# Performance work log

Hardware: AMD Instinct MI355X
Metric: run time of the kernel (lower is better)

Reference implementation:

```python
import jax, jax.numpy as jnp
import numpy as np
from jax import lax

ULB_LEN = 50000  # hardcoded ulb_dest_len in Cluster.__init__
EPS = 1e-8       # torch.cosine_similarity eps


def _l2norm(x):
    n = jnp.sqrt(jnp.sum(x * x, axis=-1, keepdims=True))
    return x / jnp.maximum(n, EPS)


def setup_inputs() -> dict:
    key = jax.random.key(0)
    k1, k2, k3, k4, k5 = jax.random.split(key, 5)
    B, C, D, K = 32768, 1000, 256, 16
    return {
        "feature": jax.random.normal(k1, (B, D), dtype=jnp.float32),
        "pred": jax.random.normal(k2, (B, C), dtype=jnp.float32),
        "centroids": jax.random.normal(k3, (C, D), dtype=jnp.float32),
        "pred_top_N": jax.random.uniform(k4, (C, K), dtype=jnp.float32),
        "unlabeled_index": jax.random.randint(k5, (B,), 0, ULB_LEN, dtype=jnp.int64),
    }


def reference(feature, pred, centroids, pred_top_N, unlabeled_index):
    B = feature.shape[0]
    C, K = pred_top_N.shape

    # batched cosine similarity to centroids -> argmax label, max cos
    cos = _l2norm(feature) @ _l2norm(centroids).T          # [B, C]
    label = jnp.argmax(cos, axis=1)                        # [B]
    cos_f = jnp.max(cos, axis=1)                           # [B]

    # confidence scores from softmax(pred)
    scores = jnp.max(jax.nn.softmax(pred, axis=1), axis=1)  # [B]

    # per-class mean / unbiased variance of cos_f (torch.var default unbiased)
    ones = jnp.ones((B,), dtype=cos_f.dtype)
    cnt = jax.ops.segment_sum(ones, label, num_segments=C)
    s1 = jax.ops.segment_sum(cos_f, label, num_segments=C)
    s2 = jax.ops.segment_sum(cos_f * cos_f, label, num_segments=C)
    mean = s1 / jnp.maximum(cnt, 1.0)
    var = (s2 - cnt * mean * mean) / jnp.maximum(cnt - 1.0, 1.0)
    std = jnp.sqrt(jnp.maximum(var, 0.0) + 1e-12)

    # weight[i] = normal(mean, std).pdf(cos_f[i]) if cos_f[i] < mean[label] else 1
    m_i, s_i = mean[label], std[label]
    inv_sqrt_2pi = 1.0 / jnp.sqrt(2.0 * jnp.pi).astype(cos_f.dtype)
    pdf = jnp.exp(-0.5 * ((cos_f - m_i) / s_i) ** 2) * inv_sqrt_2pi / s_i
    weight = jnp.where(cos_f < m_i, pdf, jnp.ones_like(cos_f))

    # sequential top-N scatter-insert into pred_top_N / fake_index
    fake_index = jnp.full((C, K), -1, dtype=jnp.int32)

    def step(carry, xs):
        topN, fidx = carry
        lb, sc, ui = xs
        row = topN[lb]                       # [K]
        mi = jnp.argmin(row)
        mv = row[mi]
        do = sc > mv
        topN = topN.at[lb, mi].set(jnp.where(do, sc, mv))
        fidx = fidx.at[lb, mi].set(jnp.where(do, ui.astype(jnp.int32), fidx[lb, mi]))
        return (topN, fidx), None

    (topN, fidx), _ = lax.scan(
        step, (pred_top_N, fake_index),
        (label, scores, unlabeled_index))

    # selected_label scatter (all samples selected: select==1 everywhere)
    selected_label = jnp.full((ULB_LEN,), -1, dtype=jnp.int32)
    selected_label = selected_label.at[unlabeled_index].set(label.astype(jnp.int32))

    return label.astype(jnp.float32), weight, topN, fidx, selected_label
```

## Files before the change

### kernel.cpp

```cpp
#include <hip/hip_runtime.h>
#include <cstdint>
#include <cstddef>

#define B_N   32768
#define C_N   1000
#define C_PAD 1024
#define D_N   256
#define K_N   16
#define ULB_N 50000
#define NCHUNK 128
#define CAP_L 128

#define OFF_L 0
#define OFF_W 32768
#define OFF_T 65536
#define OFF_F 81536
#define OFF_S 97536

typedef __attribute__((ext_vector_type(8))) short short8;
typedef __attribute__((ext_vector_type(4))) float f32x4;

__device__ __forceinline__ unsigned ordf(float f) {
  unsigned u = __float_as_uint(f);
  return (u & 0x80000000u) ? ~u : (u | 0x80000000u);
}
__device__ __forceinline__ float iordf(unsigned h) {
  unsigned u = (h & 0x80000000u) ? (h & 0x7FFFFFFFu) : ~h;
  return __uint_as_float(u);
}
__device__ __forceinline__ unsigned short f2bf(float f) {
  unsigned u = __float_as_uint(f);
  return (unsigned short)((u + 0x7FFFu + ((u >> 16) & 1u)) >> 16);
}
__device__ __forceinline__ float bf2f(unsigned short h) {
  return __uint_as_float(((unsigned)h) << 16);
}

__global__ void k_init(unsigned long long* keys, float* s1, float* s2,
                       int* cnt, int* besti) {
  int i = blockIdx.x * blockDim.x + threadIdx.x;
  if (i < B_N)  keys[i] = 0ull;
  if (i < C_PAD) { s1[i] = 0.f; s2[i] = 0.f; cnt[i] = 0; }
  if (i < ULB_N) besti[i] = -1;
}

__global__ __launch_bounds__(256) void k_pack(const float* __restrict__ src,
                                              short8* __restrict__ dst,
                                              int mt0, int nreal) {
  __shared__ float s[16][260];
  __shared__ float part[16][16];
  __shared__ float dv[16];
  const int t = threadIdx.x;
  const int mtL = blockIdx.x;
  const int r = t >> 4, c4 = (t & 15) * 4;
  const int grow = (mt0 + mtL) * 16 + r;
  #pragma unroll
  for (int i = 0; i < 4; ++i) {
    float4 v;
    if (grow < nreal) v = *reinterpret_cast<const float4*>(&src[(size_t)grow * D_N + c4 + 64 * i]);
    else { v.x = 0.f; v.y = 0.f; v.z = 0.f; v.w = 0.f; }
    s[r][c4 + 64 * i + 0] = v.x; s[r][c4 + 64 * i + 1] = v.y;
    s[r][c4 + 64 * i + 2] = v.z; s[r][c4 + 64 * i + 3] = v.w;
  }
  __syncthreads();
  {
    int c0 = t & 15;
    float ss = 0.f;
    #pragma unroll
    for (int j = 0; j < 16; ++j) { float x = s[r][c0 + 16 * j]; ss += x * x; }
    part[r][c0] = ss;
  }
  __syncthreads();
  if (t < 16) {
    float ss = 0.f;
    #pragma unroll
    for (int j = 0; j < 16; ++j) ss += part[t][j];
    dv[t] = 1.0f / fmaxf(sqrtf(ss), 1e-8f);
  }
  __syncthreads();
  #pragma unroll
  for (int i = 0; i < 4; ++i) {
    int p = t + 256 * i;
    int si = p >> 6, l = p & 63;
    int mr = l & 15, g = l >> 4;
    int kc = (si & 7) * 32 + g * 8;
    bool lo = si >= 8;
    float di = dv[mr];
    short8 v;
    #pragma unroll
    for (int j = 0; j < 8; ++j) {
      float q = s[mr][kc + j] * di;
      unsigned short hi = f2bf(q);
      unsigned short e = lo ? f2bf(q - bf2f(hi)) : hi;
      v[j] = (short)e;
    }
    dst[(size_t)mtL * 1024 + p] = v;
  }
}

__global__ __launch_bounds__(256, 3) void k_mfma(const short8* __restrict__ Ap,
                                                 const short8* __restrict__ Bp,
                                                 unsigned long long* __restrict__ keys,
                                                 int row0) {
  const int bid = blockIdx.x;
  const int nby = gridDim.x >> 3;
  int byl, bx;
  if ((nby & 63) == 0) {
    int xcd = bid & 7, j = bid >> 3;
    int slab = nby >> 3;
    int grp = j >> 6, jj = j & 63;
    byl = xcd * slab + grp * 8 + (jj & 7);
    bx = jj >> 3;
  } else { byl = bid >> 3; bx = bid & 7; }

  const int w = threadIdx.x >> 6, l = threadIdx.x & 63;
  const int wm = (w & 1) * 64, wn = (w >> 1) * 64;
  const short8* a0 = Ap + (size_t)(byl * 8 + (wm >> 4)) * 1024 + l;
  const short8* b0 = Bp + (size_t)(bx * 8 + (wn >> 4)) * 1024 + l;

  f32x4 acc[4][4];
  #pragma unroll
  for (int i = 0; i < 4; ++i)
    #pragma unroll
    for (int j = 0; j < 4; ++j) { acc[i][j][0] = 0.f; acc[i][j][1] = 0.f; acc[i][j][2] = 0.f; acc[i][j][3] = 0.f; }

  short8 Ah[4], Bh[4], Al[4], Bl[4];
#define MFMA16(fa, fb) { \
    _Pragma("unroll") \
    for (int mi = 0; mi < 4; ++mi) \
      _Pragma("unroll") \
      for (int nj = 0; nj < 4; ++nj) \
        acc[mi][nj] = __builtin_amdgcn_mfma_f32_16x16x32_bf16(fa[mi], fb[nj], acc[mi][nj], 0, 0, 0); }

  #pragma unroll 1
  for (int ks = 0; ks < 8; ++ks) {
    #pragma unroll
    for (int i = 0; i < 4; ++i) Ah[i] = a0[ks * 64 + i * 1024];
    #pragma unroll
    for (int i = 0; i < 4; ++i) Bh[i] = b0[ks * 64 + i * 1024];
    #pragma unroll
    for (int i = 0; i < 4; ++i) Al[i] = a0[(ks + 8) * 64 + i * 1024];
    #pragma unroll
    for (int i = 0; i < 4; ++i) Bl[i] = b0[(ks + 8) * 64 + i * 1024];
    MFMA16(Ah, Bh)
    MFMA16(Al, Bh)
    MFMA16(Ah, Bl)
  }
#undef MFMA16

  const int cb = bx * 128 + wn + (l & 15);
  #pragma unroll
  for (int mi = 0; mi < 4; ++mi) {
    #pragma unroll
    for (int r = 0; r < 4; ++r) {
      float bv = -INFINITY; int bc = 0x7FFFFFFF;
      #pragma unroll
      for (int nj = 0; nj < 4; ++nj) {
        int c = cb + nj * 16;
        float v = acc[mi][nj][r];
        if (c < C_N && v > bv) { bv = v; bc = c; }
      }
      #pragma unroll
      for (int mk = 1; mk < 16; mk <<= 1) {
        float ov = __shfl_xor(bv, mk, 64);
        int oc = __shfl_xor(bc, mk, 64);
        if (ov > bv || (ov == bv && oc < bc)) { bv = ov; bc = oc; }
      }
      if ((l & 15) == 0) {
        unsigned long long kk =
            (((unsigned long long)ordf(bv)) << 32) |
            (unsigned long long)(0xFFFFFFFFu - (unsigned)bc);
        atomicMax(&keys[row0 + byl * 128 + wm + mi * 16 + (l >> 4) * 4 + r], kk);
      }
    }
  }
}

__global__ __launch_bounds__(256) void k_scores(const float* __restrict__ pred,
                                                float* __restrict__ scores) {
  __shared__ float red[8];
  int r = blockIdx.x, t = threadIdx.x;
  const float* row = pred + (size_t)r * C_N;
  float x0 = row[t];
  float x1 = row[256 + t];
  float x2 = row[512 + t];
  bool v3 = (768 + t) < C_N;
  float x3 = v3 ? row[768 + t] : -INFINITY;
  float m = fmaxf(fmaxf(x0, x1), fmaxf(x2, x3));
  #pragma unroll
  for (int mk = 1; mk < 64; mk <<= 1) m = fmaxf(m, __shfl_xor(m, mk, 64));
  int wid = t >> 6, lane = t & 63;
  if (lane == 0) red[wid] = m;
  __syncthreads();
  m = fmaxf(fmaxf(red[0], red[1]), fmaxf(red[2], red[3]));
  float s = expf(x0 - m) + expf(x1 - m) + expf(x2 - m) + (v3 ? expf(x3 - m) : 0.f);
  #pragma unroll
  for (int mk = 1; mk < 64; mk <<= 1) s += __shfl_xor(s, mk, 64);
  __syncthreads();
  if (lane == 0) red[4 + wid] = s;
  __syncthreads();
  if (t == 0) {
    float S = ((red[4] + red[5]) + red[6]) + red[7];
    scores[r] = 1.0f / S;
  }
}

__global__ void k_post(const unsigned long long* __restrict__ keys, const int* __restrict__ ui,
                       int* __restrict__ labels, float* __restrict__ cosf_,
                       float* __restrict__ s1, float* __restrict__ s2, int* __restrict__ cnt,
                       int* __restrict__ besti, float* __restrict__ out) {
  int b = blockIdx.x * blockDim.x + threadIdx.x;
  if (b >= B_N) return;
  unsigned long long k = keys[b];
  int c = (int)(0xFFFFFFFFu - (unsigned)k);
  float f = iordf((unsigned)(k >> 32));
  labels[b] = c;
  cosf_[b] = f;
  out[OFF_L + b] = (float)c;
  atomicAdd(&s1[c], f);
  atomicAdd(&s2[c], f * f);
  atomicAdd(&cnt[c], 1);
  atomicMax(&besti[ui[b]], b);
}

__global__ __launch_bounds__(256) void k_hist_rank(const int* __restrict__ labels,
                                                   unsigned short* __restrict__ lrank,
                                                   unsigned short* __restrict__ hist) {
  __shared__ int lab[256];
  __shared__ unsigned histl[C_PAD];
  int chunk = blockIdx.x, t = threadIdx.x;
  int b = chunk * 256 + t;
  #pragma unroll
  for (int r = 0; r < 4; ++r) histl[t + 256 * r] = 0;
  int c = labels[b];
  lab[t] = c;
  __syncthreads();
  atomicAdd(&histl[c], 1u);
  unsigned rk = 0;
  for (int j = 0; j < t; ++j) rk += (lab[j] == c);
  lrank[b] = (unsigned short)rk;
  __syncthreads();
  #pragma unroll
  for (int r = 0; r < 4; ++r)
    hist[chunk * C_PAD + t + 256 * r] = (unsigned short)histl[t + 256 * r];
}

__global__ void k_prefix(const unsigned short* __restrict__ hist,
                         unsigned short* __restrict__ base,
                         int* __restrict__ class_n) {
  int c = blockIdx.x * 64 + threadIdx.x;
  unsigned run = 0;
  for (int t = 0; t < NCHUNK; ++t) {
    unsigned h = hist[t * C_PAD + c];
    base[t * C_PAD + c] = (unsigned short)run;
    run += h;
  }
  class_n[c] = (int)run;
}

__global__ __launch_bounds__(256) void k_sw(const int* __restrict__ labels,
                                            const unsigned short* __restrict__ lrank,
                                            const unsigned short* __restrict__ base,
                                            const float* __restrict__ scores,
                                            const int* __restrict__ ui,
                                            const float* __restrict__ cosf_,
                                            const float* __restrict__ s1,
                                            const float* __restrict__ s2,
                                            const int* __restrict__ cnt,
                                            float* __restrict__ lists_s,
                                            int* __restrict__ lists_u,
                                            float* __restrict__ out) {
  int b = blockIdx.x * blockDim.x + threadIdx.x;
  if (b >= B_N) return;
  int c = labels[b];
  int chunk = b >> 8;
  int pos = (int)base[chunk * C_PAD + c] + (int)lrank[b];
  if (pos < CAP_L) {
    lists_s[c * CAP_L + pos] = scores[b];
    lists_u[c * CAP_L + pos] = ui[b];
  }
  float n = (float)cnt[c];
  float m = s1[c] / fmaxf(n, 1.0f);
  float var = (s2[c] - n * m * m) / fmaxf(n - 1.0f, 1.0f);
  float sd = sqrtf(fmaxf(var, 0.0f) + 1e-12f);
  float cf = cosf_[b];
  float wgt = 1.0f;
  if (cf < m) {
    float z = (cf - m) / sd;
    const float inv = 0.3989422804014327f;
    wgt = expf(-0.5f * (z * z)) * inv / sd;
  }
  out[OFF_W + b] = wgt;
}

__global__ __launch_bounds__(256) void k_replay(const float* __restrict__ ptn,
                                                const float* __restrict__ lists_s,
                                                const int* __restrict__ lists_u,
                                                const int* __restrict__ class_n,
                                                const int* __restrict__ labels,
                                                const float* __restrict__ scores,
                                                const int* __restrict__ ui,
                                                float* __restrict__ out) {
  int c = blockIdx.x * 4 + (threadIdx.x >> 6);
  int lane = threadIdx.x & 63;
  if (c >= C_N) return;

  float tv[K_N]; int fi[K_N];
  #pragma unroll
  for (int j = 0; j < K_N; ++j) { tv[j] = ptn[c * K_N + j]; fi[j] = -1; }

  auto ins = [&](float s, int u) {
    float mv = tv[0]; int mi = 0;
    #pragma unroll
    for (int j = 1; j < K_N; ++j) { if (tv[j] < mv) { mv = tv[j]; mi = j; } }
    if (s > mv) {
      #pragma unroll
      for (int j = 0; j < K_N; ++j) { if (j == mi) { tv[j] = s; fi[j] = u; } }
    }
  };

  int n = class_n[c];
  if (n <= CAP_L) {
    for (int t0 = 0; t0 < n; t0 += 64) {
      float s = 0.f; int u = 0;
      int idx = t0 + lane;
      if (idx < n) { s = lists_s[c * CAP_L + idx]; u = lists_u[c * CAP_L + idx]; }
      int lim = min(64, n - t0);
      for (int t = 0; t < lim; ++t) {
        float ss = __shfl(s, t, 64);
        int uu = __shfl(u, t, 64);
        ins(ss, uu);
      }
    }
  } else {
    for (int t0 = 0; t0 < B_N; t0 += 64) {
      int lb = labels[t0 + lane];
      unsigned long long match = __ballot(lb == c);
      while (match) {
        int t = __ffsll((long long)match) - 1;
        match &= match - 1;
        int b = t0 + t;
        ins(scores[b], ui[b]);
      }
    }
  }

  if (lane == 0) {
    #pragma unroll
    for (int j = 0; j < K_N; ++j) {
      out[OFF_T + c * K_N + j] = tv[j];
      out[OFF_F + c * K_N + j] = (float)fi[j];
    }
  }
}

__global__ void k_sel(const int* __restrict__ besti, const int* __restrict__ labels,
                      float* __restrict__ out) {
  int p = blockIdx.x * blockDim.x + threadIdx.x;
  if (p >= ULB_N) return;
  int bi = besti[p];
  out[OFF_S + p] = (bi < 0) ? -1.0f : (float)labels[bi];
}

extern "C" void kernel_launch(void* const* d_in, const int* in_sizes, int n_in,
                              void* d_out, int out_size, void* d_ws, size_t ws_size,
                              hipStream_t stream) {
  const float* feat = (const float*)d_in[0];
  const float* pred = (const float*)d_in[1];
  const float* cent = (const float*)d_in[2];
  const float* ptn  = (const float*)d_in[3];
  const int*   ui   = (const int*)d_in[4];
  float* out = (float*)d_out;
  char* ws = (char*)d_ws;

  size_t o = 0;
  auto alloc = [&](size_t bytes) { void* p = ws + o; o += (bytes + 255) & ~size_t(255); return p; };
  short8* Bp                = (short8*)alloc(64 * 1024 * 16);
  unsigned long long* keys  = (unsigned long long*)alloc(B_N * 8);
  int*   labels             = (int*)  alloc(B_N * 4);
  float* scores             = (float*)alloc(B_N * 4);
  float* cosf_              = (float*)alloc(B_N * 4);
  float* s1                 = (float*)alloc(C_PAD * 4);
  float* s2                 = (float*)alloc(C_PAD * 4);
  int*   cnt                = (int*)  alloc(C_PAD * 4);
  int*   besti              = (int*)  alloc(ULB_N * 4);
  unsigned short* lrank     = (unsigned short*)alloc(B_N * 2);
  unsigned short* hist      = (unsigned short*)alloc(NCHUNK * C_PAD * 2);
  unsigned short* base      = (unsigned short*)alloc(NCHUNK * C_PAD * 2);
  int*   class_n            = (int*)  alloc(C_PAD * 4);
  float* lists_s            = (float*)alloc(C_N * CAP_L * 4);
  int*   lists_u            = (int*)  alloc(C_N * CAP_L * 4);

  size_t avail = (ws_size > o) ? ws_size - o : 0;
  int g128 = (int)(avail / 131072ull);
  if (g128 < 1) g128 = 1;
  if (g128 > 256) g128 = 256;
  if (g128 >= 64) g128 &= ~63;
  else if (g128 >= 8) g128 &= ~7;
  short8* Achunk = (short8*)(ws + o);

  k_init     <<<196, 256, 0, stream>>>(keys, s1, s2, cnt, besti);
  k_pack     <<<64, 256, 0, stream>>>(cent, Bp, 0, C_N);
  for (int c0 = 0; c0 < 256; c0 += g128) {
    int g = (g128 < 256 - c0) ? g128 : (256 - c0);
    k_pack   <<<g * 8, 256, 0, stream>>>(feat, Achunk, c0 * 8, B_N);
    k_mfma   <<<g * 8, 256, 0, stream>>>(Achunk, Bp, keys, c0 * 128);
  }
  k_scores   <<<B_N, 256, 0, stream>>>(pred, scores);
  k_post     <<<B_N / 256, 256, 0, stream>>>(keys, ui, labels, cosf_, s1, s2, cnt, besti, out);
  k_hist_rank<<<NCHUNK, 256, 0, stream>>>(labels, lrank, hist);
  k_prefix   <<<16, 64, 0, stream>>>(hist, base, class_n);
  k_sw       <<<B_N / 256, 256, 0, stream>>>(labels, lrank, base, scores, ui, cosf_, s1, s2, cnt, lists_s, lists_u, out);
  k_replay   <<<250, 256, 0, stream>>>(ptn, lists_s, lists_u, class_n, labels, scores, ui, out);
  k_sel      <<<(ULB_N + 255) / 256, 256, 0, stream>>>(besti, labels, out);
}
```

Baseline: 157.0 us.

## Fuse small kernels, double-buffer MFMA loads, vectorize softmax score reads

Merges init with centroid packing, post with histogram/rank, and the selected-label scatter into the weight kernel, cutting three kernel launches and one extra pass over labels. The MFMA loop now double-buffers its global fragment loads so the next k-step's loads overlap the current MFMAs, and launch bounds drop from 3 to 2 blocks per CU to give room for the extra registers. The score kernel reads each pred row with float4 loads. Lower occupancy could hurt latency hiding, and the fused post kernel adds shared-memory histogram work to every block.

New measurement: 161.9 us. +3.1%, slower.

```diff
diff --git a/kernel.cpp b/kernel.cpp
--- a/kernel.cpp
+++ b/kernel.cpp
@@ -36,22 +36,13 @@
   return __uint_as_float(((unsigned)h) << 16);
 }
 
-__global__ void k_init(unsigned long long* keys, float* s1, float* s2,
-                       int* cnt, int* besti) {
-  int i = blockIdx.x * blockDim.x + threadIdx.x;
-  if (i < B_N)  keys[i] = 0ull;
-  if (i < C_PAD) { s1[i] = 0.f; s2[i] = 0.f; cnt[i] = 0; }
-  if (i < ULB_N) besti[i] = -1;
-}
-
-__global__ __launch_bounds__(256) void k_pack(const float* __restrict__ src,
-                                              short8* __restrict__ dst,
-                                              int mt0, int nreal) {
+__device__ __forceinline__ void pack_body(const float* __restrict__ src,
+                                          short8* __restrict__ dst,
+                                          int mtL, int mt0, int nreal) {
   __shared__ float s[16][260];
   __shared__ float part[16][16];
   __shared__ float dv[16];
   const int t = threadIdx.x;
-  const int mtL = blockIdx.x;
   const int r = t >> 4, c4 = (t & 15) * 4;
   const int grow = (mt0 + mtL) * 16 + r;
   #pragma unroll
@@ -98,7 +89,24 @@
   }
 }
 
-__global__ __launch_bounds__(256, 3) void k_mfma(const short8* __restrict__ Ap,
+__global__ __launch_bounds__(256) void k_initpack(const float* __restrict__ cent,
+                                                  short8* __restrict__ Bp,
+                                                  unsigned long long* keys, float* s1, float* s2,
+                                                  int* cnt, int* besti) {
+  int i = blockIdx.x * blockDim.x + threadIdx.x;
+  if (i < B_N)  keys[i] = 0ull;
+  if (i < C_PAD) { s1[i] = 0.f; s2[i] = 0.f; cnt[i] = 0; }
+  if (i < ULB_N) besti[i] = -1;
+  if (blockIdx.x < 64) pack_body(cent, Bp, blockIdx.x, 0, C_N);
+}
+
+__global__ __launch_bounds__(256) void k_pack(const float* __restrict__ src,
+                                              short8* __restrict__ dst,
+                                              int mt0, int nreal) {
+  pack_body(src, dst, blockIdx.x, mt0, nreal);
+}
+
+__global__ __launch_bounds__(256, 2) void k_mfma(const short8* __restrict__ Ap,
                                                  const short8* __restrict__ Bp,
                                                  unsigned long long* __restrict__ keys,
                                                  int row0) {
@@ -124,29 +132,36 @@
     #pragma unroll
     for (int j = 0; j < 4; ++j) { acc[i][j][0] = 0.f; acc[i][j][1] = 0.f; acc[i][j][2] = 0.f; acc[i][j][3] = 0.f; }
 
-  short8 Ah[4], Bh[4], Al[4], Bl[4];
+  short8 A0h[4], B0h[4], A0l[4], B0l[4];
+  short8 A1h[4], B1h[4], A1l[4], B1l[4];
+#define LOADSET(Xh, Yh, Xl, Yl, ks) { \
+    _Pragma("unroll") \
+    for (int i = 0; i < 4; ++i) Xh[i] = a0[(ks) * 64 + i * 1024]; \
+    _Pragma("unroll") \
+    for (int i = 0; i < 4; ++i) Yh[i] = b0[(ks) * 64 + i * 1024]; \
+    _Pragma("unroll") \
+    for (int i = 0; i < 4; ++i) Xl[i] = a0[((ks) + 8) * 64 + i * 1024]; \
+    _Pragma("unroll") \
+    for (int i = 0; i < 4; ++i) Yl[i] = b0[((ks) + 8) * 64 + i * 1024]; }
 #define MFMA16(fa, fb) { \
     _Pragma("unroll") \
     for (int mi = 0; mi < 4; ++mi) \
       _Pragma("unroll") \
       for (int nj = 0; nj < 4; ++nj) \
         acc[mi][nj] = __builtin_amdgcn_mfma_f32_16x16x32_bf16(fa[mi], fb[nj], acc[mi][nj], 0, 0, 0); }
-
+#define MFMA48(Xh, Yh, Xl, Yl) { MFMA16(Xh, Yh) MFMA16(Xl, Yh) MFMA16(Xh, Yl) }
+
+  LOADSET(A0h, B0h, A0l, B0l, 0)
   #pragma unroll 1
-  for (int ks = 0; ks < 8; ++ks) {
-    #pragma unroll
-    for (int i = 0; i < 4; ++i) Ah[i] = a0[ks * 64 + i * 1024];
-    #pragma unroll
-    for (int i = 0; i < 4; ++i) Bh[i] = b0[ks * 64 + i * 1024];
-    #pragma unroll
-    for (int i = 0; i < 4; ++i) Al[i] = a0[(ks + 8) * 64 + i * 1024];
-    #pragma unroll
-    for (int i = 0; i < 4; ++i) Bl[i] = b0[(ks + 8) * 64 + i * 1024];
-    MFMA16(Ah, Bh)
-    MFMA16(Al, Bh)
-    MFMA16(Ah, Bl)
-  }
+  for (int ks = 0; ks < 8; ks += 2) {
+    LOADSET(A1h, B1h, A1l, B1l, ks + 1)
+    MFMA48(A0h, B0h, A0l, B0l)
+    if (ks + 2 < 8) LOADSET(A0h, B0h, A0l, B0l, ks + 2)
+    MFMA48(A1h, B1h, A1l, B1l)
+  }
+#undef LOADSET
 #undef MFMA16
+#undef MFMA48
 
   const int cb = bx * 128 + wn + (l & 15);
   #pragma unroll
@@ -181,19 +196,18 @@
   __shared__ float red[8];
   int r = blockIdx.x, t = threadIdx.x;
   const float* row = pred + (size_t)r * C_N;
-  float x0 = row[t];
-  float x1 = row[256 + t];
-  float x2 = row[512 + t];
-  bool v3 = (768 + t) < C_N;
-  float x3 = v3 ? row[768 + t] : -INFINITY;
-  float m = fmaxf(fmaxf(x0, x1), fmaxf(x2, x3));
+  float4 v;
+  bool act = t < 250;
+  if (act) v = *reinterpret_cast<const float4*>(&row[t * 4]);
+  else { v.x = -INFINITY; v.y = -INFINITY; v.z = -INFINITY; v.w = -INFINITY; }
+  float m = fmaxf(fmaxf(v.x, v.y), fmaxf(v.z, v.w));
   #pragma unroll
   for (int mk = 1; mk < 64; mk <<= 1) m = fmaxf(m, __shfl_xor(m, mk, 64));
   int wid = t >> 6, lane = t & 63;
   if (lane == 0) red[wid] = m;
   __syncthreads();
   m = fmaxf(fmaxf(red[0], red[1]), fmaxf(red[2], red[3]));
-  float s = expf(x0 - m) + expf(x1 - m) + expf(x2 - m) + (v3 ? expf(x3 - m) : 0.f);
+  float s = act ? expf(v.x - m) + expf(v.y - m) + expf(v.z - m) + expf(v.w - m) : 0.f;
   #pragma unroll
   for (int mk = 1; mk < 64; mk <<= 1) s += __shfl_xor(s, mk, 64);
   __syncthreads();
@@ -205,12 +219,20 @@
   }
 }
 
-__global__ void k_post(const unsigned long long* __restrict__ keys, const int* __restrict__ ui,
-                       int* __restrict__ labels, float* __restrict__ cosf_,
-                       float* __restrict__ s1, float* __restrict__ s2, int* __restrict__ cnt,
-                       int* __restrict__ besti, float* __restrict__ out) {
-  int b = blockIdx.x * blockDim.x + threadIdx.x;
-  if (b >= B_N) return;
+__global__ __launch_bounds__(256) void k_post(const unsigned long long* __restrict__ keys,
+                                              const int* __restrict__ ui,
+                                              int* __restrict__ labels, float* __restrict__ cosf_,
+                                              float* __restrict__ s1, float* __restrict__ s2,
+                                              int* __restrict__ cnt, int* __restrict__ besti,
+                                              unsigned short* __restrict__ lrank,
+                                              unsigned short* __restrict__ hist,
+                                              float* __restrict__ out) {
+  __shared__ int lab[256];
+  __shared__ unsigned histl[C_PAD];
+  int chunk = blockIdx.x, t = threadIdx.x;
+  int b = chunk * 256 + t;
+  #pragma unroll
+  for (int r = 0; r < 4; ++r) histl[t + 256 * r] = 0;
   unsigned long long k = keys[b];
   int c = (int)(0xFFFFFFFFu - (unsigned)k);
   float f = iordf((unsigned)(k >> 32));
@@ -221,18 +243,6 @@
   atomicAdd(&s2[c], f * f);
   atomicAdd(&cnt[c], 1);
   atomicMax(&besti[ui[b]], b);
-}
-
-__global__ __launch_bounds__(256) void k_hist_rank(const int* __restrict__ labels,
-                                                   unsigned short* __restrict__ lrank,
-                                                   unsigned short* __restrict__ hist) {
-  __shared__ int lab[256];
-  __shared__ unsigned histl[C_PAD];
-  int chunk = blockIdx.x, t = threadIdx.x;
-  int b = chunk * 256 + t;
-  #pragma unroll
-  for (int r = 0; r < 4; ++r) histl[t + 256 * r] = 0;
-  int c = labels[b];
   lab[t] = c;
   __syncthreads();
   atomicAdd(&histl[c], 1u);
@@ -267,6 +277,7 @@
                                             const float* __restrict__ s1,
                                             const float* __restrict__ s2,
                                             const int* __restrict__ cnt,
+                                            const int* __restrict__ besti,
                                             float* __restrict__ lists_s,
                                             int* __restrict__ lists_u,
                                             float* __restrict__ out) {
@@ -291,6 +302,15 @@
     wgt = expf(-0.5f * (z * z)) * inv / sd;
   }
   out[OFF_W + b] = wgt;
+  {
+    int bi = besti[b];
+    out[OFF_S + b] = (bi < 0) ? -1.0f : (float)labels[bi];
+  }
+  int p2 = b + B_N;
+  if (p2 < ULB_N) {
+    int bi = besti[p2];
+    out[OFF_S + p2] = (bi < 0) ? -1.0f : (float)labels[bi];
+  }
 }
 
 __global__ __launch_bounds__(256) void k_replay(const float* __restrict__ ptn,
@@ -352,14 +372,6 @@
       out[OFF_F + c * K_N + j] = (float)fi[j];
     }
   }
-}
-
-__global__ void k_sel(const int* __restrict__ besti, const int* __restrict__ labels,
-                      float* __restrict__ out) {
-  int p = blockIdx.x * blockDim.x + threadIdx.x;
-  if (p >= ULB_N) return;
-  int bi = besti[p];
-  out[OFF_S + p] = (bi < 0) ? -1.0f : (float)labels[bi];
 }
 
 extern "C" void kernel_launch(void* const* d_in, const int* in_sizes, int n_in,
@@ -399,18 +411,15 @@
   else if (g128 >= 8) g128 &= ~7;
   short8* Achunk = (short8*)(ws + o);
 
-  k_init     <<<196, 256, 0, stream>>>(keys, s1, s2, cnt, besti);
-  k_pack     <<<64, 256, 0, stream>>>(cent, Bp, 0, C_N);
+  k_initpack <<<196, 256, 0, stream>>>(cent, Bp, keys, s1, s2, cnt, besti);
   for (int c0 = 0; c0 < 256; c0 += g128) {
     int g = (g128 < 256 - c0) ? g128 : (256 - c0);
     k_pack   <<<g * 8, 256, 0, stream>>>(feat, Achunk, c0 * 8, B_N);
     k_mfma   <<<g * 8, 256, 0, stream>>>(Achunk, Bp, keys, c0 * 128);
   }
   k_scores   <<<B_N, 256, 0, stream>>>(pred, scores);
-  k_post     <<<B_N / 256, 256, 0, stream>>>(keys, ui, labels, cosf_, s1, s2, cnt, besti, out);
-  k_hist_rank<<<NCHUNK, 256, 0, stream>>>(labels, lrank, hist);
+  k_post     <<<NCHUNK, 256, 0, stream>>>(keys, ui, labels, cosf_, s1, s2, cnt, besti, lrank, hist, out);
   k_prefix   <<<16, 64, 0, stream>>>(hist, base, class_n);
-  k_sw       <<<B_N / 256, 256, 0, stream>>>(labels, lrank, base, scores, ui, cosf_, s1, s2, cnt, lists_s, lists_u, out);
+  k_sw       <<<B_N / 256, 256, 0, stream>>>(labels, lrank, base, scores, ui, cosf_, s1, s2, cnt, besti, lists_s, lists_u, out);
   k_replay   <<<250, 256, 0, stream>>>(ptn, lists_s, lists_u, class_n, labels, scores, ui, out);
-  k_sel      <<<(ULB_N + 255) / 256, 256, 0, stream>>>(besti, labels, out);
-}
+}
```
